# Kernel tuning notes

Measured on AMD Instinct MI355X. Metric: run time of the kernel, lower is better.

The kernel has to match this reference:

```python
import jax, jax.numpy as jnp
import numpy as np

NUM_POINTS = 500_000
NUM_SUP = 8192
DEGREE = 32
HIDDEN = 256
NDIM = 3


def sincos_embed(coords, dim):
    # Faithful port of kappamodules ContinuousSincosEmbed.
    ndim = coords.shape[-1]
    ndim_padding = dim % ndim
    dim_per = (dim - ndim_padding) // ndim
    sincos_padding = dim_per % 2
    padding = ndim_padding + sincos_padding * ndim
    eff = (dim - padding) // ndim  # even
    omega = 1.0 / (10000.0 ** (jnp.arange(0, eff, 2, dtype=jnp.float32) / eff))
    out = coords[..., None] * omega  # (N, ndim, eff//2)
    emb = jnp.concatenate([jnp.sin(out), jnp.cos(out)], axis=-1)  # (N, ndim, eff)
    emb = emb.reshape(coords.shape[:-1] + (ndim * eff,))
    if padding > 0:
        emb = jnp.pad(emb, [(0, 0)] * (emb.ndim - 1) + [(0, padding)])
    return emb


def setup_inputs() -> dict:
    key = jax.random.key(0)
    ks = jax.random.split(key, 8)
    input_pos = jax.random.uniform(ks[0], (NUM_POINTS, NDIM), dtype=jnp.float32)
    supernode_idx = jnp.sort(
        jax.random.randint(ks[1], (NUM_SUP,), 0, NUM_POINTS, dtype=jnp.int32)
    )
    src_idx = jax.random.randint(ks[2], (NUM_SUP * DEGREE,), 0, NUM_POINTS, dtype=jnp.int32)
    dst_seg = jnp.repeat(jnp.arange(NUM_SUP, dtype=jnp.int32), DEGREE)
    s = 1.0 / np.sqrt(HIDDEN)
    w1 = jax.random.normal(ks[3], (HIDDEN, HIDDEN), dtype=jnp.float32) * s
    w2 = jax.random.normal(ks[4], (HIDDEN, HIDDEN), dtype=jnp.float32) * s
    wp = jax.random.normal(ks[5], (2 * HIDDEN, HIDDEN), dtype=jnp.float32) / np.sqrt(2 * HIDDEN)
    b1 = jnp.zeros((HIDDEN,), jnp.float32)
    b2 = jnp.zeros((HIDDEN,), jnp.float32)
    bp = jnp.zeros((HIDDEN,), jnp.float32)
    return {
        "input_pos": input_pos, "supernode_idx": supernode_idx,
        "src_idx": src_idx, "dst_seg": dst_seg,
        "w1": w1, "b1": b1, "w2": w2, "b2": b2, "wp": wp, "bp": bp,
    }


def reference(input_pos, supernode_idx, src_idx, dst_seg, w1, b1, w2, b2, wp, bp):
    num_sup = supernode_idx.shape[0]
    sup_pos = input_pos[supernode_idx]            # (S, 3)
    src_pos = input_pos[src_idx]                  # (E, 3)
    dst_pos = sup_pos[dst_seg]                    # (E, 3)
    dist = dst_pos - src_pos
    mag = jnp.linalg.norm(dist, axis=1, keepdims=True)
    rel = jnp.concatenate([dist, mag], axis=1)    # (E, 4)
    x = sincos_embed(rel, HIDDEN)                 # (E, H) relpos embed, ndim=4
    # message MLP: Linear -> GELU(exact) -> Linear
    x = jax.nn.gelu(x @ w1 + b1, approximate=False) @ w2 + b2
    # segment mean into supernodes (dst is sorted/consecutive per supernode)
    sums = jax.ops.segment_sum(x, dst_seg, num_segments=num_sup)
    counts = jax.ops.segment_sum(jnp.ones((x.shape[0],), x.dtype), dst_seg, num_segments=num_sup)
    agg = sums / jnp.maximum(counts, 1.0)[:, None]  # (S, H)
    sup_embed = sincos_embed(sup_pos, HIDDEN)       # (S, H) abspos embed, ndim=3
    out = jnp.concatenate([agg, sup_embed], axis=-1) @ wp + bp  # (S, H)
    return out[None]  # (1, S, H) -- batch_size=1 (batch_idx=None)
```

## Files before the change

kernel.cpp:

```cpp
#include <hip/hip_runtime.h>
#include <hip/hip_bf16.h>

typedef __bf16 bf16_t;
typedef bf16_t bf16x8 __attribute__((ext_vector_type(8)));
typedef float f32x16 __attribute__((ext_vector_type(16)));

constexpr float OMG[16] = {
    1.0f,        0.74989421f, 0.56234133f, 0.42169650f,
    0.31622777f, 0.23713737f, 0.17782794f, 0.13335214f,
    0.1f,        0.074989421f, 0.056234133f, 0.042169650f,
    0.031622777f, 0.023713737f, 0.017782794f, 0.013335214f};

__device__ __forceinline__ f32x16 mfma_bf16(bf16x8 a, bf16x8 b, f32x16 c) {
  return __builtin_amdgcn_mfma_f32_32x32x16_bf16(a, b, c, 0, 0, 0);
}

__device__ __forceinline__ int orig_k(int pk) {
  return 64 * (pk >> 5) + 32 * ((pk >> 4) & 1) + (pk & 15);
}

__global__ __launch_bounds__(256) void prep(
    const float* __restrict__ w1, const float* __restrict__ w2,
    const float* __restrict__ wp, const float* __restrict__ b1,
    const float* __restrict__ b2, const float* __restrict__ bp,
    const float* __restrict__ pos, const int* __restrict__ sup_idx,
    bf16_t* __restrict__ w1img, bf16_t* __restrict__ wpT2,
    float* __restrict__ bfold, float* __restrict__ b1fold,
    bf16_t* __restrict__ cat) {
  __shared__ float T[256][33];
  const int bid = blockIdx.x;
  const int tid = threadIdx.x;

  if (bid < 8) {
    const int n0 = bid * 32;
#pragma unroll
    for (int it = 0; it < 16; ++it) {
      const int pk = it * 8 + (tid >> 5);
      T[pk][tid & 31] = w1[orig_k(pk) * 256 + n0 + (tid & 31)];
    }
    __syncthreads();
    const int n_off = tid & 31;
    const int n = n0 + n_off;
#pragma unroll
    for (int q = 0; q < 2; ++q) {
      const int slot = (tid >> 5) + 8 * q;
      bf16x8 v;
#pragma unroll
      for (int e = 0; e < 8; ++e) v[e] = (bf16_t)T[slot * 8 + e][n_off];
      *(bf16x8*)((char*)w1img + n * 256 + ((slot ^ (n & 15)) << 4)) = v;
    }
  } else if (bid == 8) {
    const int n = tid;
    float vl[4];
    float bf1 = b1[n];
#pragma unroll
    for (int d = 0; d < 4; ++d) {
      float s = 0.f;
#pragma unroll
      for (int i = 0; i < 16; ++i)
        s = fmaf(0.01f * OMG[i], w1[(64 * d + 16 + i) * 256 + n], s);
      vl[d] = s;
#pragma unroll
      for (int i = 0; i < 16; ++i) bf1 += w1[(64 * d + 48 + i) * 256 + n];
    }
    bf16_t* ext = w1img + 32768 + n * 16;
#pragma unroll
    for (int e = 0; e < 4; ++e) ext[e] = (bf16_t)vl[e];
#pragma unroll
    for (int e = 4; e < 16; ++e) ext[e] = (bf16_t)0.0f;
    b1fold[n] = bf1;
  } else if (bid < 17) {
    const int band = (bid - 9) * 32;
#pragma unroll
    for (int it = 0; it < 32; ++it)
      T[tid][it] = wp[(256 + band + it) * 256 + tid];
    __syncthreads();
    const int o = tid;
#pragma unroll
    for (int g = 0; g < 4; ++g) {
      bf16x8 v;
#pragma unroll
      for (int e = 0; e < 8; ++e) v[e] = (bf16_t)T[o][g * 8 + e];
      *(bf16x8*)(wpT2 + o * 512 + 256 + band + g * 8) = v;
    }
  } else if (bid < 81) {
    const int t2 = bid - 17;
    const int o0 = (t2 >> 3) * 32, j0 = (t2 & 7) * 32;
#pragma unroll
    for (int it = 0; it < 32; ++it) {
      const int n = it * 8 + (tid >> 5);
      T[n][tid & 31] = wp[n * 256 + o0 + (tid & 31)];
    }
    __syncthreads();
    const int o_off = tid & 31, jb = tid >> 5;
    float a4[4] = {0.f, 0.f, 0.f, 0.f};
    for (int n = 0; n < 256; ++n) {
      const float wv = T[n][o_off];
#pragma unroll
      for (int q = 0; q < 4; ++q)
        a4[q] = fmaf(w2[(j0 + jb + 8 * q) * 256 + n], wv, a4[q]);
    }
#pragma unroll
    for (int q = 0; q < 4; ++q)
      wpT2[(o0 + o_off) * 512 + j0 + jb + 8 * q] = (bf16_t)a4[q];
  } else if (bid < 337) {
    const int col = tid;
    int d = 0, sc2 = 0;
    float om = 0.0f;
    if (col < 252) {
      d = (col >= 84 ? 1 : 0) + (col >= 168 ? 1 : 0);
      const int t3 = col - 84 * d;
      sc2 = (t3 >= 42) ? 1 : 0;
      om = __expf(-0.21929381838038533f * (float)(t3 - 42 * sc2));
    }
    const int r0 = (bid - 81) * 32;
    for (int it = 0; it < 32; ++it) {
      const int row = r0 + it;
      float v = 0.0f;
      if (col < 252) {
        const float a = pos[sup_idx[row] * 3 + d] * om;
        v = sc2 ? __cosf(a) : __sinf(a);
      }
      cat[row * 512 + 256 + col] = (bf16_t)v;
    }
  } else {
    const int o = (bid - 337) * 8 + (tid >> 5);
    const int kl = (tid & 31) * 8;
    float s = 0.f;
#pragma unroll
    for (int k = 0; k < 8; ++k) s += b2[kl + k] * wp[(kl + k) * 256 + o];
    s += __shfl_xor(s, 16); s += __shfl_xor(s, 8); s += __shfl_xor(s, 4);
    s += __shfl_xor(s, 2); s += __shfl_xor(s, 1);
    if ((tid & 31) == 0) bfold[o] = s + bp[o];
  }
}

__global__ __launch_bounds__(512, 2) void edge_mlp(
    const float* __restrict__ pos, const int* __restrict__ sup_idx,
    const int* __restrict__ src_idx,
    const bf16_t* __restrict__ w1img, const float* __restrict__ b1fold,
    bf16_t* __restrict__ cat) {
  __shared__ __attribute__((aligned(16))) bf16_t Bs[36864];

  const int tid = threadIdx.x;

  {
    const bf16x8* src8 = (const bf16x8*)w1img;
    bf16x8* dst8 = (bf16x8*)Bs;
#pragma unroll
    for (int it = 0; it < 9; ++it) {
      const int idx = it * 512 + tid;
      dst8[idx] = src8[idx];
    }
  }

  const int l = tid & 63, w = tid >> 6;
  const int hi = l >> 5, lc = l & 31;
  const int s = blockIdx.x * 8 + w;

  const int si = sup_idx[s];
  const int srci = src_idx[s * 32 + lc];
  const float dx = pos[si * 3 + 0] - pos[srci * 3 + 0];
  const float dy = pos[si * 3 + 1] - pos[srci * 3 + 1];
  const float dz = pos[si * 3 + 2] - pos[srci * 3 + 2];
  const float mg = sqrtf(dx * dx + dy * dy + dz * dz);
  const float rv[4] = {dx, dy, dz, mg};

  float omg[8];
#pragma unroll
  for (int e = 0; e < 8; ++e) omg[e] = hi ? OMG[8 + e] : OMG[e];

  __syncthreads();

  f32x16 acc[8];
#pragma unroll
  for (int nt = 0; nt < 8; ++nt)
#pragma unroll
    for (int p = 0; p < 16; ++p) acc[nt][p] = 0.0f;

  const char* Bb = (const char*)Bs;

  {
    bf16x8 aext;
#pragma unroll
    for (int e = 0; e < 8; ++e)
      aext[e] = (hi == 0 && e < 4) ? (bf16_t)rv[e] : (bf16_t)0.0f;
    const char* eb = Bb + 65536 + lc * 32 + hi * 16;
#pragma unroll
    for (int nt = 0; nt < 8; ++nt) {
      bf16x8 be = *(const bf16x8*)(eb + nt * 1024);
      acc[nt] = mfma_bf16(aext, be, acc[nt]);
    }
  }

  const int sxor = (lc & 15) << 4;
  const int rowb = lc * 256;

#pragma unroll
  for (int d = 0; d < 4; ++d) {
    float ang[8];
#pragma unroll
    for (int e = 0; e < 8; ++e) ang[e] = rv[d] * omg[e];
    bf16x8 a_sin, a_cos;
#pragma unroll
    for (int e = 0; e < 8; ++e) a_sin[e] = (bf16_t)__sinf(ang[e]);
#pragma unroll
    for (int e = 0; e < 8; ++e) a_cos[e] = (bf16_t)__cosf(ang[e]);

    const int ko_sin = ((4 * d + hi) << 4) ^ sxor;
    const int ko_cos = ((4 * d + 2 + hi) << 4) ^ sxor;
#pragma unroll
    for (int g = 0; g < 2; ++g) {
      bf16x8 b0 = *(const bf16x8*)(Bb + rowb + (4 * g + 0) * 8192 + ko_sin);
      bf16x8 b1_ = *(const bf16x8*)(Bb + rowb + (4 * g + 1) * 8192 + ko_sin);
      bf16x8 b2_ = *(const bf16x8*)(Bb + rowb + (4 * g + 2) * 8192 + ko_sin);
      bf16x8 b3 = *(const bf16x8*)(Bb + rowb + (4 * g + 3) * 8192 + ko_sin);
      acc[4 * g + 0] = mfma_bf16(a_sin, b0, acc[4 * g + 0]);
      acc[4 * g + 1] = mfma_bf16(a_sin, b1_, acc[4 * g + 1]);
      acc[4 * g + 2] = mfma_bf16(a_sin, b2_, acc[4 * g + 2]);
      acc[4 * g + 3] = mfma_bf16(a_sin, b3, acc[4 * g + 3]);
    }
#pragma unroll
    for (int g = 0; g < 2; ++g) {
      bf16x8 b0 = *(const bf16x8*)(Bb + rowb + (4 * g + 0) * 8192 + ko_cos);
      bf16x8 b1_ = *(const bf16x8*)(Bb + rowb + (4 * g + 1) * 8192 + ko_cos);
      bf16x8 b2_ = *(const bf16x8*)(Bb + rowb + (4 * g + 2) * 8192 + ko_cos);
      bf16x8 b3 = *(const bf16x8*)(Bb + rowb + (4 * g + 3) * 8192 + ko_cos);
      acc[4 * g + 0] = mfma_bf16(a_cos, b0, acc[4 * g + 0]);
      acc[4 * g + 1] = mfma_bf16(a_cos, b1_, acc[4 * g + 1]);
      acc[4 * g + 2] = mfma_bf16(a_cos, b2_, acc[4 * g + 2]);
      acc[4 * g + 3] = mfma_bf16(a_cos, b3, acc[4 * g + 3]);
    }
  }

  const float C2 = -0.10296644f, C0 = -2.3022765f;
#pragma unroll
  for (int nt = 0; nt < 8; ++nt) {
    const float bi = b1fold[32 * nt + lc];
    float ssum = 0.0f;
#pragma unroll
    for (int p = 0; p < 16; p += 2) {
      const float x0 = acc[nt][p] + bi;
      const float x1 = acc[nt][p + 1] + bi;
      const float u0 = x0 * x0, u1 = x1 * x1;
      const float t0 = fmaf(u0, C2, C0), t1 = fmaf(u1, C2, C0);
      const float v0 = x0 * t0, v1 = x1 * t1;
      const float e0 = exp2f(v0), e1 = exp2f(v1);
      const float d0 = e0 + 1.0f, d1 = e1 + 1.0f;
      const float r0 = __builtin_amdgcn_rcpf(d0);
      const float r1 = __builtin_amdgcn_rcpf(d1);
      ssum = fmaf(x0, r0, ssum);
      ssum = fmaf(x1, r1, ssum);
    }
    ssum += __shfl_xor(ssum, 32);
    if (hi == 0) cat[s * 512 + 32 * nt + lc] = (bf16_t)(ssum * 0.03125f);
  }
}

__global__ __launch_bounds__(256) void proj(
    const bf16_t* __restrict__ cat, const bf16_t* __restrict__ wpT2,
    const float* __restrict__ bfold, float* __restrict__ out) {
  const int tid = threadIdx.x;
  const int l = tid & 63, w = tid >> 6;
  const int hi = l >> 5, lc = l & 31;
  const int rm = blockIdx.x * 32;
  const int cn = blockIdx.y * 128 + w * 32;
  const int r0 = rm + lc;
  const int c0 = cn + lc;

  f32x16 a0;
#pragma unroll
  for (int p = 0; p < 16; ++p) a0[p] = 0.f;
#pragma unroll 8
  for (int kk = 0; kk < 32; ++kk) {
    int k0 = kk * 16 + 8 * hi;
    bf16x8 fa0 = *(const bf16x8*)(cat + r0 * 512 + k0);
    bf16x8 fb = *(const bf16x8*)(wpT2 + c0 * 512 + k0);
    a0 = mfma_bf16(fa0, fb, a0);
  }
  float bias = bfold[c0];
#pragma unroll
  for (int rr = 0; rr < 16; ++rr) {
    int rowo = (rr & 3) + 8 * (rr >> 2) + 4 * hi;
    out[(rm + rowo) * 256 + c0] = a0[rr] + bias;
  }
}

extern "C" void kernel_launch(void* const* d_in, const int* in_sizes, int n_in,
                              void* d_out, int out_size, void* d_ws, size_t ws_size,
                              hipStream_t stream) {
  const float* pos = (const float*)d_in[0];
  const int* sup_idx = (const int*)d_in[1];
  const int* src_idx = (const int*)d_in[2];
  const float* w1 = (const float*)d_in[4];
  const float* b1 = (const float*)d_in[5];
  const float* w2 = (const float*)d_in[6];
  const float* b2 = (const float*)d_in[7];
  const float* wp = (const float*)d_in[8];
  const float* bp = (const float*)d_in[9];

  char* ws = (char*)d_ws;
  bf16_t* w1img = (bf16_t*)(ws);
  bf16_t* wpT2  = (bf16_t*)(ws + 73728);
  float*  bfold = (float*)(ws + 335872);
  float*  b1fold = (float*)(ws + 336896);
  bf16_t* cat   = (bf16_t*)(ws + 337920);
  float* out = (float*)d_out;

  if (ws_size < (size_t)(337920 + 8192 * 512 * 2)) return;

  prep<<<dim3(369), dim3(256), 0, stream>>>(
      w1, w2, wp, b1, b2, bp, pos, sup_idx, w1img, wpT2, bfold, b1fold, cat);
  edge_mlp<<<dim3(1024), dim3(512), 0, stream>>>(pos, sup_idx, src_idx, w1img, b1fold, cat);
  proj<<<dim3(256, 2), dim3(256), 0, stream>>>(cat, wpT2, bfold, out);
}
```

Measured before the change: 78.97 us.

## Move supernode sincos embed into edge kernel, fold bias, widen proj tile

The supernode absolute-position sincos embedding moves out of the prep kernel (which shrinks from 369 to 114 blocks) and into the edge_mlp tail. It is computed from a small omega/phase table, with cosine written as a phase-shifted sine. The b1 bias now initialises the accumulators instead of being added after the matmul, and the GELU epilogue is written with two-wide float vectors to invite packed math. The proj kernel computes 64 rows per block with two MFMA accumulators sharing each weight fragment. The intent is to shorten the prep critical path and cut launch and weight-load cost, at the price of extra epilogue work in edge_mlp and a different, less exact cos path.

After: 68.30 us, median of 2. 13.5% less time.

```diff
diff --git a/kernel.cpp b/kernel.cpp
--- a/kernel.cpp
+++ b/kernel.cpp
@@ -4,6 +4,7 @@
 typedef __bf16 bf16_t;
 typedef bf16_t bf16x8 __attribute__((ext_vector_type(8)));
 typedef float f32x16 __attribute__((ext_vector_type(16)));
+typedef float f32x2 __attribute__((ext_vector_type(2)));
 
 constexpr float OMG[16] = {
     1.0f,        0.74989421f, 0.56234133f, 0.42169650f,
@@ -23,10 +24,9 @@
     const float* __restrict__ w1, const float* __restrict__ w2,
     const float* __restrict__ wp, const float* __restrict__ b1,
     const float* __restrict__ b2, const float* __restrict__ bp,
-    const float* __restrict__ pos, const int* __restrict__ sup_idx,
     bf16_t* __restrict__ w1img, bf16_t* __restrict__ wpT2,
     float* __restrict__ bfold, float* __restrict__ b1fold,
-    bf16_t* __restrict__ cat) {
+    f32x2* __restrict__ ometab, int* __restrict__ dtab) {
   __shared__ float T[256][33];
   const int bid = blockIdx.x;
   const int tid = threadIdx.x;
@@ -103,28 +103,8 @@
 #pragma unroll
     for (int q = 0; q < 4; ++q)
       wpT2[(o0 + o_off) * 512 + j0 + jb + 8 * q] = (bf16_t)a4[q];
-  } else if (bid < 337) {
-    const int col = tid;
-    int d = 0, sc2 = 0;
-    float om = 0.0f;
-    if (col < 252) {
-      d = (col >= 84 ? 1 : 0) + (col >= 168 ? 1 : 0);
-      const int t3 = col - 84 * d;
-      sc2 = (t3 >= 42) ? 1 : 0;
-      om = __expf(-0.21929381838038533f * (float)(t3 - 42 * sc2));
-    }
-    const int r0 = (bid - 81) * 32;
-    for (int it = 0; it < 32; ++it) {
-      const int row = r0 + it;
-      float v = 0.0f;
-      if (col < 252) {
-        const float a = pos[sup_idx[row] * 3 + d] * om;
-        v = sc2 ? __cosf(a) : __sinf(a);
-      }
-      cat[row * 512 + 256 + col] = (bf16_t)v;
-    }
-  } else {
-    const int o = (bid - 337) * 8 + (tid >> 5);
+  } else if (bid < 113) {
+    const int o = (bid - 81) * 8 + (tid >> 5);
     const int kl = (tid & 31) * 8;
     float s = 0.f;
 #pragma unroll
@@ -132,6 +112,20 @@
     s += __shfl_xor(s, 16); s += __shfl_xor(s, 8); s += __shfl_xor(s, 4);
     s += __shfl_xor(s, 2); s += __shfl_xor(s, 1);
     if ((tid & 31) == 0) bfold[o] = s + bp[o];
+  } else {
+    const int col = tid;
+    float om = 0.0f, ph = 0.0f;
+    int d = 0;
+    if (col < 252) {
+      d = (col >= 84 ? 1 : 0) + (col >= 168 ? 1 : 0);
+      const int t3 = col - 84 * d;
+      const int sc2 = (t3 >= 42) ? 1 : 0;
+      om = __expf(-0.21929381838038533f * (float)(t3 - 42 * sc2));
+      ph = sc2 ? 1.57079632679f : 0.0f;
+    }
+    f32x2 op; op[0] = om; op[1] = ph;
+    ometab[col] = op;
+    dtab[col] = d;
   }
 }
 
@@ -139,6 +133,7 @@
     const float* __restrict__ pos, const int* __restrict__ sup_idx,
     const int* __restrict__ src_idx,
     const bf16_t* __restrict__ w1img, const float* __restrict__ b1fold,
+    const f32x2* __restrict__ ometab, const int* __restrict__ dtab,
     bf16_t* __restrict__ cat) {
   __shared__ __attribute__((aligned(16))) bf16_t Bs[36864];
 
@@ -174,9 +169,11 @@
 
   f32x16 acc[8];
 #pragma unroll
-  for (int nt = 0; nt < 8; ++nt)
-#pragma unroll
-    for (int p = 0; p < 16; ++p) acc[nt][p] = 0.0f;
+  for (int nt = 0; nt < 8; ++nt) {
+    const float bi = b1fold[32 * nt + lc];
+#pragma unroll
+    for (int p = 0; p < 16; ++p) acc[nt][p] = bi;
+  }
 
   const char* Bb = (const char*)Bs;
 
@@ -233,27 +230,37 @@
     }
   }
 
-  const float C2 = -0.10296644f, C0 = -2.3022765f;
+  const f32x2 C2v = {-0.10296644f, -0.10296644f};
+  const f32x2 C0v = {-2.3022765f, -2.3022765f};
 #pragma unroll
   for (int nt = 0; nt < 8; ++nt) {
-    const float bi = b1fold[32 * nt + lc];
-    float ssum = 0.0f;
+    f32x2 ss2 = {0.0f, 0.0f};
 #pragma unroll
     for (int p = 0; p < 16; p += 2) {
-      const float x0 = acc[nt][p] + bi;
-      const float x1 = acc[nt][p + 1] + bi;
-      const float u0 = x0 * x0, u1 = x1 * x1;
-      const float t0 = fmaf(u0, C2, C0), t1 = fmaf(u1, C2, C0);
-      const float v0 = x0 * t0, v1 = x1 * t1;
-      const float e0 = exp2f(v0), e1 = exp2f(v1);
-      const float d0 = e0 + 1.0f, d1 = e1 + 1.0f;
-      const float r0 = __builtin_amdgcn_rcpf(d0);
-      const float r1 = __builtin_amdgcn_rcpf(d1);
-      ssum = fmaf(x0, r0, ssum);
-      ssum = fmaf(x1, r1, ssum);
-    }
+      f32x2 x; x[0] = acc[nt][p]; x[1] = acc[nt][p + 1];
+      f32x2 u = x * x;
+      f32x2 t = u * C2v + C0v;
+      f32x2 v = x * t;
+      f32x2 e; e[0] = exp2f(v[0]); e[1] = exp2f(v[1]);
+      f32x2 den = e + 1.0f;
+      f32x2 r;
+      r[0] = __builtin_amdgcn_rcpf(den[0]);
+      r[1] = __builtin_amdgcn_rcpf(den[1]);
+      ss2 = x * r + ss2;
+    }
+    float ssum = ss2[0] + ss2[1];
     ssum += __shfl_xor(ssum, 32);
     if (hi == 0) cat[s * 512 + 32 * nt + lc] = (bf16_t)(ssum * 0.03125f);
+  }
+
+#pragma unroll
+  for (int q = 0; q < 4; ++q) {
+    const int col = 64 * q + l;
+    const f32x2 op = ometab[col];
+    const int d = dtab[col];
+    const float pd = pos[si * 3 + d];
+    const float v = __sinf(fmaf(pd, op[0], op[1]));
+    cat[s * 512 + 256 + col] = (bf16_t)v;
   }
 }
 
@@ -263,26 +270,29 @@
   const int tid = threadIdx.x;
   const int l = tid & 63, w = tid >> 6;
   const int hi = l >> 5, lc = l & 31;
-  const int rm = blockIdx.x * 32;
+  const int rm = blockIdx.x * 64;
   const int cn = blockIdx.y * 128 + w * 32;
-  const int r0 = rm + lc;
+  const int r0 = rm + lc, r1 = rm + 32 + lc;
   const int c0 = cn + lc;
 
-  f32x16 a0;
-#pragma unroll
-  for (int p = 0; p < 16; ++p) a0[p] = 0.f;
+  f32x16 a0, a1;
+#pragma unroll
+  for (int p = 0; p < 16; ++p) { a0[p] = 0.f; a1[p] = 0.f; }
 #pragma unroll 8
   for (int kk = 0; kk < 32; ++kk) {
     int k0 = kk * 16 + 8 * hi;
     bf16x8 fa0 = *(const bf16x8*)(cat + r0 * 512 + k0);
+    bf16x8 fa1 = *(const bf16x8*)(cat + r1 * 512 + k0);
     bf16x8 fb = *(const bf16x8*)(wpT2 + c0 * 512 + k0);
     a0 = mfma_bf16(fa0, fb, a0);
+    a1 = mfma_bf16(fa1, fb, a1);
   }
   float bias = bfold[c0];
 #pragma unroll
   for (int rr = 0; rr < 16; ++rr) {
     int rowo = (rr & 3) + 8 * (rr >> 2) + 4 * hi;
     out[(rm + rowo) * 256 + c0] = a0[rr] + bias;
+    out[(rm + 32 + rowo) * 256 + c0] = a1[rr] + bias;
   }
 }
 
@@ -300,17 +310,20 @@
   const float* bp = (const float*)d_in[9];
 
   char* ws = (char*)d_ws;
-  bf16_t* w1img = (bf16_t*)(ws);
-  bf16_t* wpT2  = (bf16_t*)(ws + 73728);
-  float*  bfold = (float*)(ws + 335872);
+  bf16_t* w1img  = (bf16_t*)(ws);
+  bf16_t* wpT2   = (bf16_t*)(ws + 73728);
+  float*  bfold  = (float*)(ws + 335872);
   float*  b1fold = (float*)(ws + 336896);
-  bf16_t* cat   = (bf16_t*)(ws + 337920);
+  f32x2*  ometab = (f32x2*)(ws + 337920);
+  int*    dtab   = (int*)(ws + 339968);
+  bf16_t* cat    = (bf16_t*)(ws + 340992);
   float* out = (float*)d_out;
 
-  if (ws_size < (size_t)(337920 + 8192 * 512 * 2)) return;
-
-  prep<<<dim3(369), dim3(256), 0, stream>>>(
-      w1, w2, wp, b1, b2, bp, pos, sup_idx, w1img, wpT2, bfold, b1fold, cat);
-  edge_mlp<<<dim3(1024), dim3(512), 0, stream>>>(pos, sup_idx, src_idx, w1img, b1fold, cat);
-  proj<<<dim3(256, 2), dim3(256), 0, stream>>>(cat, wpT2, bfold, out);
-}
+  if (ws_size < (size_t)(340992 + 8192 * 512 * 2)) return;
+
+  prep<<<dim3(114), dim3(256), 0, stream>>>(
+      w1, w2, wp, b1, b2, bp, w1img, wpT2, bfold, b1fold, ometab, dtab);
+  edge_mlp<<<dim3(1024), dim3(512), 0, stream>>>(
+      pos, sup_idx, src_idx, w1img, b1fold, ometab, dtab, cat);
+  proj<<<dim3(128, 2), dim3(256), 0, stream>>>(cat, wpT2, bfold, out);
+}
```
